# Optimization experiments

Measured on AMD Instinct MI355X. Metric: run time of the kernel, lower is better.

The kernel has to match this reference:

```python
import jax, jax.numpy as jnp
import numpy as np

B, T, C = 2, 2048, 2048
H = 16
HD = C // H
MLP_DIM = 4 * C
EPS = 1e-5


def rmsnorm(x):
    return x * jax.lax.rsqrt(jnp.mean(x * x, axis=-1, keepdims=True) + EPS)


def setup_inputs() -> dict:
    key = jax.random.key(0)
    ks = jax.random.split(key, 7)
    s = 0.02
    return {
        "x": jax.random.normal(ks[0], (B, T, C), dtype=jnp.float32),
        "wq": jax.random.normal(ks[1], (C, C), dtype=jnp.float32) * s,
        "wk": jax.random.normal(ks[2], (C, C), dtype=jnp.float32) * s,
        "wv": jax.random.normal(ks[3], (C, C), dtype=jnp.float32) * s,
        "wo": jax.random.normal(ks[4], (C, C), dtype=jnp.float32) * s,
        "fc1": jax.random.normal(ks[5], (MLP_DIM, C), dtype=jnp.float32) * s,
        "fc2": jax.random.normal(ks[6], (C, MLP_DIM), dtype=jnp.float32) * s,
    }


def reference(x, wq, wk, wv, wo, fc1, fc2):
    # --- attention sub-block (pre-norm) ---
    h = rmsnorm(x)
    # nn.Linear applies x @ W.T
    q = (h @ wq.T).reshape(B, T, H, HD).transpose(0, 2, 1, 3)  # [B,H,T,HD]
    k = (h @ wk.T).reshape(B, T, H, HD).transpose(0, 2, 1, 3)
    v = (h @ wv.T).reshape(B, T, H, HD).transpose(0, 2, 1, 3)
    scale = 1.0 / np.sqrt(HD)
    scores = jnp.einsum("bhqd,bhkd->bhqk", q, k) * scale
    causal_mask = jnp.triu(jnp.full((T, T), -jnp.inf, dtype=scores.dtype), k=1)
    scores = scores + causal_mask
    attn = jax.nn.softmax(scores, axis=-1)
    out = jnp.einsum("bhqk,bhkd->bhqd", attn, v)
    out = out.transpose(0, 2, 1, 3).reshape(B, T, C)
    x = x + out @ wo.T
    # --- MLP sub-block (squared ReLU) ---
    h = rmsnorm(x)
    m = h @ fc1.T
    m = jnp.square(jax.nn.relu(m))
    x = x + m @ fc2.T
    return x
```

## Files before the change

### kernel.cpp

```cpp
#include <hip/hip_runtime.h>


typedef __bf16 bf16x8 __attribute__((ext_vector_type(8)));
typedef __bf16 bf16x4 __attribute__((ext_vector_type(4)));
typedef float  f32x4  __attribute__((ext_vector_type(4)));

static __device__ __forceinline__ __bf16 tobf(float f) { return (__bf16)f; }

static __device__ __forceinline__ void async_copy16(const void* g, void* l) {
    __builtin_amdgcn_global_load_lds(
        (const __attribute__((address_space(1))) void*)g,
        (__attribute__((address_space(3))) void*)l, 16, 0, 0);
}

#define LGKM0_FENCE()  asm volatile("s_waitcnt lgkmcnt(0)" ::: "memory")
#define VMCNT8_FENCE() asm volatile("s_waitcnt vmcnt(8)" ::: "memory")
#define VMCNT0_FENCE() asm volatile("s_waitcnt vmcnt(0)" ::: "memory")
#define CFENCE()       asm volatile("" ::: "memory")

__global__ void detect_dtype_kernel(const unsigned short* __restrict__ xh,
                                    int* __restrict__ flag) {
    int t = threadIdx.x;
    unsigned short u = xh[2 * t];
    int e = (u >> 7) & 0xFF;
    bool outlier = (e < 100) || (e > 131);
    unsigned long long m = __ballot(outlier);
    if (t == 0) *flag = (__popcll(m) >= 16) ? 1 : 0;
}

__global__ __launch_bounds__(256) void convert_w4(
    const void* __restrict__ w0, const void* __restrict__ w1,
    const void* __restrict__ w2, const void* __restrict__ w3,
    __bf16* __restrict__ dqkvo, const int* __restrict__ flagp) {
    constexpr size_t CC = (size_t)2048 * 2048;
    const int y = blockIdx.y;
    size_t i = ((size_t)blockIdx.x * 256 + threadIdx.x) * 8;
    const void* s = (y == 0) ? w0 : (y == 1) ? w1 : (y == 2) ? w2 : w3;
    __bf16* d = dqkvo + (size_t)y * CC;
    if (*flagp != 0) {
        const float4* sp = (const float4*)((const float*)s + i);
        float4 a = sp[0], b = sp[1];
        bf16x8 o = {tobf(a.x), tobf(a.y), tobf(a.z), tobf(a.w),
                    tobf(b.x), tobf(b.y), tobf(b.z), tobf(b.w)};
        *(bf16x8*)(d + i) = o;
    } else {
        *(bf16x8*)(d + i) = *(const bf16x8*)((const __bf16*)s + i);
    }
}

__global__ __launch_bounds__(256) void convert_w1(
    const void* __restrict__ src, __bf16* __restrict__ dst,
    const int* __restrict__ flagp) {
    size_t i = ((size_t)blockIdx.x * 256 + threadIdx.x) * 8;
    if (*flagp != 0) {
        const float4* sp = (const float4*)((const float*)src + i);
        float4 a = sp[0], b = sp[1];
        bf16x8 o = {tobf(a.x), tobf(a.y), tobf(a.z), tobf(a.w),
                    tobf(b.x), tobf(b.y), tobf(b.z), tobf(b.w)};
        *(bf16x8*)(dst + i) = o;
    } else {
        *(bf16x8*)(dst + i) = *(const bf16x8*)((const __bf16*)src + i);
    }
}

template <int SRC>
__global__ __launch_bounds__(256) void rmsnorm_kernel(
    const void* __restrict__ xp, __bf16* __restrict__ h,
    const int* __restrict__ flagp) {
    constexpr int C = 2048;
    const int row = blockIdx.x, t = threadIdx.x;
    float vals[8];
    bool f32in = (SRC == 1) || (*flagp != 0);
    if (f32in) {
        const float4* xr = (const float4*)((const float*)xp + (size_t)row * C);
        float4 a = xr[2 * t], b = xr[2 * t + 1];
        vals[0] = a.x; vals[1] = a.y; vals[2] = a.z; vals[3] = a.w;
        vals[4] = b.x; vals[5] = b.y; vals[6] = b.z; vals[7] = b.w;
    } else {
        bf16x8 a = *((const bf16x8*)((const __bf16*)xp + (size_t)row * C) + t);
#pragma unroll
        for (int j = 0; j < 8; ++j) vals[j] = (float)a[j];
    }
    float ss = 0.f;
#pragma unroll
    for (int j = 0; j < 8; ++j) ss += vals[j] * vals[j];
#pragma unroll
    for (int off = 32; off > 0; off >>= 1) ss += __shfl_down(ss, off);
    __shared__ float red[4];
    if ((t & 63) == 0) red[t >> 6] = ss;
    __syncthreads();
    float mean = (red[0] + red[1] + red[2] + red[3]) * (1.0f / C);
    float sc = rsqrtf(mean + 1e-5f);
    bf16x8 o;
#pragma unroll
    for (int j = 0; j < 8; ++j) o[j] = tobf(vals[j] * sc);
    *((bf16x8*)(h + (size_t)row * C) + t) = o;
}

static __device__ __forceinline__ void gemm_core_128pf(
    const __bf16* __restrict__ A, const __bf16* __restrict__ W,
    int m0, int n0, int K,
    __bf16 (*As)[128][64], __bf16 (*Bs)[128][64], f32x4 (&acc)[4][4]) {
    const int t = threadIdx.x;
    const int wave = t >> 6, lane = t & 63;
    const int lr = lane & 15, lq = lane >> 4;
    const int wm = wave & 1, wn = wave >> 1;
    const int sx = lr & 7;
    const int NT = K >> 6;

    const __bf16* gA[4];
    const __bf16* gB[4];
    int lo[4];
#pragma unroll
    for (int i = 0; i < 4; ++i) {
        int c = i * 256 + t;
        int row = c >> 3;
        int sl = (c & 7) ^ (row & 7);
        gA[i] = A + (size_t)(m0 + row) * K + sl * 8;
        gB[i] = W + (size_t)(n0 + row) * K + sl * 8;
        lo[i] = (c & ~63) * 8;
    }

    const f32x4 zero = {0.f, 0.f, 0.f, 0.f};
#pragma unroll
    for (int i = 0; i < 4; ++i)
#pragma unroll
        for (int j = 0; j < 4; ++j) acc[i][j] = zero;

#pragma unroll
    for (int i = 0; i < 4; ++i) {
        async_copy16(gA[i], &As[0][0][0] + lo[i]);
        async_copy16(gB[i], &Bs[0][0][0] + lo[i]);
    }

    for (int tt = 0; tt < NT; ++tt) {
        const int cur = tt & 1;
        if (tt + 1 < NT) {
            const int k1 = (tt + 1) * 64;
#pragma unroll
            for (int i = 0; i < 4; ++i) {
                async_copy16(gA[i] + k1, &As[cur ^ 1][0][0] + lo[i]);
                async_copy16(gB[i] + k1, &Bs[cur ^ 1][0][0] + lo[i]);
            }
            VMCNT8_FENCE();
        } else {
            VMCNT0_FENCE();
        }
        __builtin_amdgcn_s_barrier();
        CFENCE();

        bf16x8 a[4][2], b[4][2];
#pragma unroll
        for (int kk = 0; kk < 2; ++kk) {
            const int sp = ((kk * 4 + lq) ^ sx) * 8;
#pragma unroll
            for (int ii = 0; ii < 4; ++ii) {
                a[ii][kk] = *(const bf16x8*)&As[cur][wm * 64 + ii * 16 + lr][sp];
                b[ii][kk] = *(const bf16x8*)&Bs[cur][wn * 64 + ii * 16 + lr][sp];
            }
        }
#pragma unroll
        for (int ii = 0; ii < 4; ++ii)
#pragma unroll
            for (int jj = 0; jj < 4; ++jj)
#pragma unroll
                for (int kk = 0; kk < 2; ++kk)
                    acc[ii][jj] = __builtin_amdgcn_mfma_f32_16x16x32_bf16(
                        a[ii][kk], b[jj][kk], acc[ii][jj], 0, 0, 0);
        CFENCE();
        __builtin_amdgcn_s_barrier();
        CFENCE();
    }
}

template <int EPI>
__global__ __launch_bounds__(256) void gemm_nt(
    const __bf16* __restrict__ A, const __bf16* __restrict__ W,
    void* __restrict__ outp, const void* __restrict__ resp,
    int M, int N, int K, const int* __restrict__ flagp) {
    __shared__ __align__(16) __bf16 As[2][128][64];
    __shared__ __align__(16) __bf16 Bs[2][128][64];
    const int t = threadIdx.x;
    const int wave = t >> 6, lane = t & 63;
    const int lr = lane & 15, lq = lane >> 4;
    const int wm = wave & 1, wn = wave >> 1;
    const int m0 = blockIdx.y * 128, n0 = blockIdx.x * 128;

    f32x4 acc[4][4];
    gemm_core_128pf(A, W, m0, n0, K, As, Bs, acc);

    const bool f32 = (*flagp != 0);
#pragma unroll
    for (int i = 0; i < 4; ++i)
#pragma unroll
        for (int j = 0; j < 4; ++j)
#pragma unroll
            for (int r = 0; r < 4; ++r) {
                int row = m0 + wm * 64 + i * 16 + lq * 4 + r;
                int col = n0 + wn * 64 + j * 16 + lr;
                size_t o = (size_t)row * N + col;
                float v = acc[i][j][r];
                if (EPI == 5) {
                    float res = f32 ? ((const float*)resp)[o]
                                    : (float)((const __bf16*)resp)[o];
                    ((float*)outp)[o] = v + res;
                } else {
                    float ov = v + ((const float*)resp)[o];
                    if (f32) ((float*)outp)[o] = ov;
                    else     ((__bf16*)outp)[o] = tobf(ov);
                }
            }
}

__global__ __launch_bounds__(256) void gemm_qkv(
    const __bf16* __restrict__ A, const __bf16* __restrict__ Wall,
    __bf16* __restrict__ qout, __bf16* __restrict__ kout,
    __bf16* __restrict__ vtout) {
    constexpr int N = 2048, K = 2048;
    constexpr float kQScale = 1.4426950408889634f * 0.08838834764831845f;
    __shared__ __align__(16) __bf16 As[2][128][64];
    __shared__ __align__(16) __bf16 Bs[2][128][64];
    const int t = threadIdx.x;
    const int wave = t >> 6, lane = t & 63;
    const int lr = lane & 15, lq = lane >> 4;
    const int wm = wave & 1, wn = wave >> 1;
    const int which = blockIdx.x >> 4;
    const int m0 = blockIdx.y * 128, n0 = (blockIdx.x & 15) * 128;
    const __bf16* W = Wall + (size_t)which * N * K;

    f32x4 acc[4][4];
    gemm_core_128pf(A, W, m0, n0, K, As, Bs, acc);

    if (which < 2) {
        __bf16* outp = (which == 0) ? qout : kout;
        const float sc = (which == 0) ? kQScale : 1.0f;
#pragma unroll
        for (int i = 0; i < 4; ++i)
#pragma unroll
            for (int j = 0; j < 4; ++j)
#pragma unroll
                for (int r = 0; r < 4; ++r) {
                    int row = m0 + wm * 64 + i * 16 + lq * 4 + r;
                    int col = n0 + wn * 64 + j * 16 + lr;
                    outp[(size_t)row * N + col] = tobf(acc[i][j][r] * sc);
                }
    } else {
#pragma unroll
        for (int i = 0; i < 4; ++i)
#pragma unroll
            for (int j = 0; j < 4; ++j) {
                int t0 = m0 + wm * 64 + i * 16 + lq * 4;
                int b  = t0 >> 11, tt = t0 & 2047;
                int col = n0 + wn * 64 + j * 16 + lr;
                bf16x4 p = {tobf(acc[i][j][0]), tobf(acc[i][j][1]),
                            tobf(acc[i][j][2]), tobf(acc[i][j][3])};
                *(bf16x4*)(vtout + (((size_t)(b * 2048 + col)) << 11) + tt) = p;
            }
    }
}

static __device__ __forceinline__ void gemm_core_256(
    const __bf16* __restrict__ A, const __bf16* __restrict__ W,
    int m0, int n0, int K,
    __bf16 (*As)[256][64], __bf16 (*Bs)[256][64], f32x4 (&acc)[8][4]) {
    const int tid = threadIdx.x;
    const int wave = tid >> 6, lane = tid & 63;
    const int lr = lane & 15, lq = lane >> 4;
    const int wm = wave >> 2, wn = wave & 3;
    const int sx = lr & 7;
    const int NT = K >> 6;

    int off[4], lo[4];
#pragma unroll
    for (int i = 0; i < 4; ++i) {
        int c = i * 512 + tid;
        int row = c >> 3;
        off[i] = row * K + (((c & 7) ^ (row & 7)) * 8);
        lo[i] = (c & ~63) * 8;
    }

    const f32x4 zero = {0.f, 0.f, 0.f, 0.f};
#pragma unroll
    for (int m = 0; m < 8; ++m)
#pragma unroll
        for (int n = 0; n < 4; ++n) acc[m][n] = zero;

#pragma unroll
    for (int pt = 0; pt < 2; ++pt) {
        const __bf16* ga = A + (size_t)m0 * K + pt * 64;
        const __bf16* gb = W + (size_t)n0 * K + pt * 64;
#pragma unroll
        for (int i = 0; i < 4; ++i)
            async_copy16(ga + off[i], &As[pt][0][0] + lo[i]);
#pragma unroll
        for (int i = 0; i < 4; ++i)
            async_copy16(gb + off[i], &Bs[pt][0][0] + lo[i]);
    }
    VMCNT8_FENCE();
    __builtin_amdgcn_s_barrier();

    for (int t = 0; t < NT; ++t) {
        const int bi = t & 1;
        const __bf16 (*Ac)[64] = As[bi];
        const __bf16 (*Bc)[64] = Bs[bi];
        const int ts = (t + 2 < NT) ? t + 2 : NT - 1;
        const __bf16* gAt = A + (size_t)m0 * K + (size_t)ts * 64;
        const __bf16* gBt = W + (size_t)n0 * K + (size_t)ts * 64;

        bf16x8 a0[4][2], a1[4][2], b0[2][2], b1[2][2];

#pragma unroll
        for (int m = 0; m < 4; ++m)
#pragma unroll
            for (int kk = 0; kk < 2; ++kk)
                a0[m][kk] = *(const bf16x8*)
                    &Ac[wm * 128 + m * 16 + lr][((kk * 4 + lq) ^ sx) * 8];
#pragma unroll
        for (int n = 0; n < 2; ++n)
#pragma unroll
            for (int kk = 0; kk < 2; ++kk)
                b0[n][kk] = *(const bf16x8*)
                    &Bc[wn * 64 + n * 16 + lr][((kk * 4 + lq) ^ sx) * 8];
        __builtin_amdgcn_s_barrier();
        LGKM0_FENCE();
        __builtin_amdgcn_s_setprio(1);
#pragma unroll
        for (int m = 0; m < 4; ++m)
#pragma unroll
            for (int n = 0; n < 2; ++n)
#pragma unroll
                for (int kk = 0; kk < 2; ++kk)
                    acc[m][n] = __builtin_amdgcn_mfma_f32_16x16x32_bf16(
                        a0[m][kk], b0[n][kk], acc[m][n], 0, 0, 0);
        __builtin_amdgcn_s_setprio(0);
        __builtin_amdgcn_s_barrier();

#pragma unroll
        for (int m = 0; m < 4; ++m)
#pragma unroll
            for (int kk = 0; kk < 2; ++kk)
                a1[m][kk] = *(const bf16x8*)
                    &Ac[wm * 128 + (m + 4) * 16 + lr][((kk * 4 + lq) ^ sx) * 8];
        __builtin_amdgcn_s_barrier();
        LGKM0_FENCE();
        __builtin_amdgcn_s_setprio(1);
#pragma unroll
        for (int m = 0; m < 4; ++m)
#pragma unroll
            for (int n = 0; n < 2; ++n)
#pragma unroll
                for (int kk = 0; kk < 2; ++kk)
                    acc[m + 4][n] = __builtin_amdgcn_mfma_f32_16x16x32_bf16(
                        a1[m][kk], b0[n][kk], acc[m + 4][n], 0, 0, 0);
        __builtin_amdgcn_s_setprio(0);
        __builtin_amdgcn_s_barrier();

#pragma unroll
        for (int n = 0; n < 2; ++n)
#pragma unroll
            for (int kk = 0; kk < 2; ++kk)
                b1[n][kk] = *(const bf16x8*)
                    &Bc[wn * 64 + (n + 2) * 16 + lr][((kk * 4 + lq) ^ sx) * 8];
#pragma unroll
        for (int i = 0; i < 4; ++i)
            async_copy16(gAt + off[i], &As[bi][0][0] + lo[i]);
        __builtin_amdgcn_s_barrier();
        LGKM0_FENCE();
        __builtin_amdgcn_s_setprio(1);
#pragma unroll
        for (int m = 0; m < 4; ++m)
#pragma unroll
            for (int n = 0; n < 2; ++n)
#pragma unroll
                for (int kk = 0; kk < 2; ++kk)
                    acc[m + 4][n + 2] = __builtin_amdgcn_mfma_f32_16x16x32_bf16(
                        a1[m][kk], b1[n][kk], acc[m + 4][n + 2], 0, 0, 0);
        __builtin_amdgcn_s_setprio(0);
        __builtin_amdgcn_s_barrier();

#pragma unroll
        for (int i = 0; i < 4; ++i)
            async_copy16(gBt + off[i], &Bs[bi][0][0] + lo[i]);
        __builtin_amdgcn_s_barrier();
        __builtin_amdgcn_s_setprio(1);
#pragma unroll
        for (int m = 0; m < 4; ++m)
#pragma unroll
            for (int n = 0; n < 2; ++n)
#pragma unroll
                for (int kk = 0; kk < 2; ++kk)
                    acc[m][n + 2] = __builtin_amdgcn_mfma_f32_16x16x32_bf16(
                        a0[m][kk], b1[n][kk], acc[m][n + 2], 0, 0, 0);
        __builtin_amdgcn_s_setprio(0);
        VMCNT8_FENCE();
        __builtin_amdgcn_s_barrier();
    }
}

template <int EPI>
__global__ __launch_bounds__(512, 1) void gemm256_nt(
    const __bf16* __restrict__ A, const __bf16* __restrict__ W,
    void* __restrict__ outp, const void* __restrict__ resp,
    int M, int N, int K, const int* __restrict__ flagp) {
    __shared__ __align__(16) __bf16 As[2][256][64];
    __shared__ __align__(16) __bf16 Bs[2][256][64];
    const int tid = threadIdx.x;
    const int wave = tid >> 6, lane = tid & 63;
    const int lr = lane & 15, lq = lane >> 4;
    const int wm = wave >> 2, wn = wave & 3;
    const int m0 = blockIdx.y * 256, n0 = blockIdx.x * 256;

    f32x4 acc[8][4];
    gemm_core_256(A, W, m0, n0, K, As, Bs, acc);

    const bool f32 = (EPI == 2) ? false : (*flagp != 0);
#pragma unroll
    for (int m = 0; m < 8; ++m)
#pragma unroll
        for (int n = 0; n < 4; ++n)
#pragma unroll
            for (int r = 0; r < 4; ++r) {
                int row = m0 + wm * 128 + m * 16 + lq * 4 + r;
                int col = n0 + wn * 64 + n * 16 + lr;
                size_t o = (size_t)row * N + col;
                float v = acc[m][n][r];
                if (EPI == 2) {
                    float rv = v > 0.f ? v : 0.f;
                    ((__bf16*)outp)[o] = tobf(rv * rv);
                } else if (EPI == 5) {
                    float res = f32 ? ((const float*)resp)[o]
                                    : (float)((const __bf16*)resp)[o];
                    ((float*)outp)[o] = v + res;
                } else {
                    float ov = v + ((const float*)resp)[o];
                    if (f32) ((float*)outp)[o] = ov;
                    else     ((__bf16*)outp)[o] = tobf(ov);
                }
            }
}

__global__ __launch_bounds__(256) void attn_kernel(
    const __bf16* __restrict__ Q, const __bf16* __restrict__ K,
    const __bf16* __restrict__ Vt, __bf16* __restrict__ O) {
    constexpr int T = 2048, C = 2048, HD = 128;
    __shared__ __align__(16) __bf16 Ks[64][136];
    __shared__ __align__(16) __bf16 Vts[128][72];
    __shared__ __align__(16) __bf16 Ps[4][16][72];
    const int t = threadIdx.x, w = t >> 6, lane = t & 63;
    const int lr = lane & 15, lq = lane >> 4;
    const int b = blockIdx.z, h = blockIdx.y;
    const __bf16* vtb = Vt + ((size_t)(b * 2048 + h * 128) << 11);
    const f32x4 zero = {0.f, 0.f, 0.f, 0.f};

    bf16x8 ones;
#pragma unroll
    for (int j = 0; j < 8; ++j) ones[j] = (lr == 0) ? (__bf16)1.0f : (__bf16)0.0f;

    for (int pass = 0; pass < 2; ++pass) {
        const int qblk = (pass == 0) ? blockIdx.x : 31 - blockIdx.x;
        const int q0 = qblk * 64;

        const int qrow = q0 + w * 16 + lr;
        const __bf16* qb = Q + (size_t)(b * T + qrow) * C + h * HD;
        bf16x8 qf[4];
#pragma unroll
        for (int s = 0; s < 4; ++s)
            qf[s] = *(const bf16x8*)(qb + s * 32 + lq * 8);

        f32x4 oacc[8], lacc = zero;
#pragma unroll
        for (int nc = 0; nc < 8; ++nc) oacc[nc] = zero;
        float m_i[4] = {-3e38f, -3e38f, -3e38f, -3e38f};

        for (int kb = 0; kb <= qblk; ++kb) {
            const int k00 = kb * 64;
#pragma unroll
            for (int i = 0; i < 4; ++i) {
                int c = t + 256 * i;
                int r = c >> 4, col = (c & 15) * 8;
                *(bf16x8*)&Ks[r][col] =
                    *(const bf16x8*)(K + (size_t)(b * T + k00 + r) * C + h * HD + col);
            }
#pragma unroll
            for (int i = 0; i < 4; ++i) {
                int c = t + 256 * i;
                int r = c >> 3, cg = (c & 7) * 8;
                *(bf16x8*)&Vts[r][cg] =
                    *(const bf16x8*)(vtb + ((size_t)r << 11) + k00 + cg);
            }
            __syncthreads();

            float pv[4][4];
#pragma unroll
            for (int jc = 0; jc < 4; ++jc) {
                f32x4 s = zero;
#pragma unroll
                for (int ks = 0; ks < 4; ++ks) {
                    bf16x8 kf = *(const bf16x8*)&Ks[jc * 16 + lr][ks * 32 + lq * 8];
                    s = __builtin_amdgcn_mfma_f32_16x16x32_bf16(qf[ks], kf, s, 0, 0, 0);
                }
#pragma unroll
                for (int r = 0; r < 4; ++r) pv[jc][r] = s[r];
            }
            if (kb == qblk) {
#pragma unroll
                for (int jc = 0; jc < 4; ++jc)
#pragma unroll
                    for (int r = 0; r < 4; ++r)
                        if (jc * 16 + lr > w * 16 + lq * 4 + r) pv[jc][r] = -3e38f;
            }
            float rmax[4];
#pragma unroll
            for (int r = 0; r < 4; ++r)
                rmax[r] = fmaxf(fmaxf(pv[0][r], pv[1][r]), fmaxf(pv[2][r], pv[3][r]));
#pragma unroll
            for (int off = 1; off < 16; off <<= 1)
#pragma unroll
                for (int r = 0; r < 4; ++r)
                    rmax[r] = fmaxf(rmax[r], __shfl_xor(rmax[r], off));
            float alpha[4];
#pragma unroll
            for (int r = 0; r < 4; ++r) {
                float mn = fmaxf(m_i[r], rmax[r]);
                alpha[r] = exp2f(m_i[r] - mn);
                m_i[r] = mn;
            }
#pragma unroll
            for (int jc = 0; jc < 4; ++jc)
#pragma unroll
                for (int r = 0; r < 4; ++r)
                    Ps[w][lq * 4 + r][jc * 16 + lr] = tobf(exp2f(pv[jc][r] - m_i[r]));
#pragma unroll
            for (int nc = 0; nc < 8; ++nc)
#pragma unroll
                for (int r = 0; r < 4; ++r) oacc[nc][r] *= alpha[r];
#pragma unroll
            for (int r = 0; r < 4; ++r) lacc[r] *= alpha[r];
            __syncthreads();

#pragma unroll
            for (int s2 = 0; s2 < 2; ++s2) {
                bf16x8 pa = *(const bf16x8*)&Ps[w][lr][s2 * 32 + lq * 8];
#pragma unroll
                for (int nc = 0; nc < 8; ++nc) {
                    bf16x8 vf = *(const bf16x8*)&Vts[nc * 16 + lr][s2 * 32 + lq * 8];
                    oacc[nc] = __builtin_amdgcn_mfma_f32_16x16x32_bf16(
                        pa, vf, oacc[nc], 0, 0, 0);
                }
                lacc = __builtin_amdgcn_mfma_f32_16x16x32_bf16(pa, ones, lacc, 0, 0, 0);
            }
            __syncthreads();
        }

        float inv[4];
#pragma unroll
        for (int r = 0; r < 4; ++r) inv[r] = 1.0f / __shfl(lacc[r], lane & 48);
#pragma unroll
        for (int nc = 0; nc < 8; ++nc)
#pragma unroll
            for (int r = 0; r < 4; ++r) {
                int row = q0 + w * 16 + lq * 4 + r;
                O[(size_t)(b * T + row) * C + h * HD + nc * 16 + lr] =
                    tobf(oacc[nc][r] * inv[r]);
            }
        __syncthreads();
    }
}

extern "C" void kernel_launch(void* const* d_in, const int* in_sizes, int n_in,
                              void* d_out, int out_size, void* d_ws, size_t ws_size,
                              hipStream_t stream) {
    const void* x   = d_in[0];
    const void* wq  = d_in[1];
    const void* wk  = d_in[2];
    const void* wv  = d_in[3];
    const void* wo  = d_in[4];
    const void* fc1 = d_in[5];
    const void* fc2 = d_in[6];
    constexpr int Bv = 2, Tv = 2048, Cv = 2048, Hv = 16, MLP = 8192;
    constexpr int M = Bv * Tv;
    constexpr size_t NE = (size_t)M * Cv;
    constexpr size_t CC = (size_t)Cv * Cv;

    char* ws = (char*)d_ws;
    int*    flag = (int*)ws;
    __bf16* h    = (__bf16*)(ws + 256);
    __bf16* qb   = h  + NE;
    __bf16* kb   = qb + NE;
    __bf16* vt   = kb + NE;
    __bf16* ao   = vt + NE;
    float*  x1   = (float*)(ao + NE);
    __bf16* mm   = (__bf16*)(x1 + NE);
    __bf16* wqkvob = mm;
    __bf16* fc1b   = qb;
    __bf16* fc2b   = vt;

    detect_dtype_kernel<<<1, 64, 0, stream>>>((const unsigned short*)x, flag);

    convert_w4<<<dim3(2048, 4), 256, 0, stream>>>(wq, wk, wv, wo, wqkvob, flag);

    rmsnorm_kernel<0><<<M, 256, 0, stream>>>(x, h, flag);

    gemm_qkv<<<dim3(48, 32), 256, 0, stream>>>(h, wqkvob, qb, kb, vt);

    attn_kernel<<<dim3(16, Hv, Bv), 256, 0, stream>>>(qb, kb, vt, ao);

    convert_w1<<<8192, 256, 0, stream>>>(fc1, fc1b, flag);

    gemm_nt<5><<<dim3(16, 32), 256, 0, stream>>>(ao, wqkvob + 3 * CC, x1, x,
                                                 M, Cv, Cv, flag);

    convert_w1<<<8192, 256, 0, stream>>>(fc2, fc2b, flag);

    rmsnorm_kernel<1><<<M, 256, 0, stream>>>(x1, h, flag);

    gemm256_nt<2><<<dim3(32, 16), 512, 0, stream>>>(h, fc1b, mm, nullptr,
                                                    M, MLP, Cv, flag);

    gemm_nt<6><<<dim3(16, 32), 256, 0, stream>>>(mm, fc2b, d_out, x1,
                                                 M, Cv, MLP, flag);
}
```

Baseline: 772.4 us.

## Prefetch attention K/V tiles into registers, swizzle GEMM block order, interleave LDS reads

In the attention kernel, the next K and V^T tiles are now loaded from global memory into registers while the current tile is being computed, then written to LDS at the start of the next iteration. The goal is to hide global load latency. The GEMM kernel remaps block IDs with a stride-8 swizzle to change which tiles run concurrently, likely for L2 or XCD locality. The GEMM inner loop now issues the MFMAs for each k-slice right after that slice's LDS fragment reads, which lowers register pressure. The register prefetch costs extra VGPRs in the attention kernel. The swizzle assumes the block count is divisible by 8.

```diff
diff --git a/kernel.cpp b/kernel.cpp
--- a/kernel.cpp
+++ b/kernel.cpp
@@ -149,24 +149,22 @@
         __builtin_amdgcn_s_barrier();
         CFENCE();
 
-        bf16x8 a[4][2], b[4][2];
 #pragma unroll
         for (int kk = 0; kk < 2; ++kk) {
             const int sp = ((kk * 4 + lq) ^ sx) * 8;
+            bf16x8 a[4], b[4];
 #pragma unroll
             for (int ii = 0; ii < 4; ++ii) {
-                a[ii][kk] = *(const bf16x8*)&As[cur][wm * 64 + ii * 16 + lr][sp];
-                b[ii][kk] = *(const bf16x8*)&Bs[cur][wn * 64 + ii * 16 + lr][sp];
-            }
+                a[ii] = *(const bf16x8*)&As[cur][wm * 64 + ii * 16 + lr][sp];
+                b[ii] = *(const bf16x8*)&Bs[cur][wn * 64 + ii * 16 + lr][sp];
+            }
+#pragma unroll
+            for (int ii = 0; ii < 4; ++ii)
+#pragma unroll
+                for (int jj = 0; jj < 4; ++jj)
+                    acc[ii][jj] = __builtin_amdgcn_mfma_f32_16x16x32_bf16(
+                        a[ii], b[jj], acc[ii][jj], 0, 0, 0);
         }
-#pragma unroll
-        for (int ii = 0; ii < 4; ++ii)
-#pragma unroll
-            for (int jj = 0; jj < 4; ++jj)
-#pragma unroll
-                for (int kk = 0; kk < 2; ++kk)
-                    acc[ii][jj] = __builtin_amdgcn_mfma_f32_16x16x32_bf16(
-                        a[ii][kk], b[jj][kk], acc[ii][jj], 0, 0, 0);
         CFENCE();
         __builtin_amdgcn_s_barrier();
         CFENCE();
@@ -184,7 +182,10 @@
     const int wave = t >> 6, lane = t & 63;
     const int lr = lane & 15, lq = lane >> 4;
     const int wm = wave & 1, wn = wave >> 1;
-    const int m0 = blockIdx.y * 128, n0 = blockIdx.x * 128;
+    const int id  = blockIdx.x + gridDim.x * blockIdx.y;
+    const int nwg = gridDim.x * gridDim.y;
+    const int swz = (id & 7) * (nwg >> 3) + (id >> 3);
+    const int m0 = (swz / gridDim.x) * 128, n0 = (swz % gridDim.x) * 128;
 
     f32x4 acc[4][4];
     gemm_core_128pf(A, W, m0, n0, K, As, Bs, acc);
@@ -452,6 +453,11 @@
     const __bf16* vtb = Vt + ((size_t)(b * 2048 + h * 128) << 11);
     const f32x4 zero = {0.f, 0.f, 0.f, 0.f};
 
+    const int kr[4] = {t >> 4, (t + 256) >> 4, (t + 512) >> 4, (t + 768) >> 4};
+    const int kc = (t & 15) * 8;
+    const int vr[4] = {t >> 3, (t + 256) >> 3, (t + 512) >> 3, (t + 768) >> 3};
+    const int vc = (t & 7) * 8;
+
     bf16x8 ones;
 #pragma unroll
     for (int j = 0; j < 8; ++j) ones[j] = (lr == 0) ? (__bf16)1.0f : (__bf16)0.0f;
@@ -472,23 +478,31 @@
         for (int nc = 0; nc < 8; ++nc) oacc[nc] = zero;
         float m_i[4] = {-3e38f, -3e38f, -3e38f, -3e38f};
 
+        bf16x8 kreg[4], vreg[4];
+#pragma unroll
+        for (int i = 0; i < 4; ++i)
+            kreg[i] = *(const bf16x8*)(K + (size_t)(b * T + kr[i]) * C + h * HD + kc);
+#pragma unroll
+        for (int i = 0; i < 4; ++i)
+            vreg[i] = *(const bf16x8*)(vtb + ((size_t)vr[i] << 11) + vc);
+
         for (int kb = 0; kb <= qblk; ++kb) {
-            const int k00 = kb * 64;
-#pragma unroll
-            for (int i = 0; i < 4; ++i) {
-                int c = t + 256 * i;
-                int r = c >> 4, col = (c & 15) * 8;
-                *(bf16x8*)&Ks[r][col] =
-                    *(const bf16x8*)(K + (size_t)(b * T + k00 + r) * C + h * HD + col);
-            }
-#pragma unroll
-            for (int i = 0; i < 4; ++i) {
-                int c = t + 256 * i;
-                int r = c >> 3, cg = (c & 7) * 8;
-                *(bf16x8*)&Vts[r][cg] =
-                    *(const bf16x8*)(vtb + ((size_t)r << 11) + k00 + cg);
-            }
+#pragma unroll
+            for (int i = 0; i < 4; ++i) *(bf16x8*)&Ks[kr[i]][kc] = kreg[i];
+#pragma unroll
+            for (int i = 0; i < 4; ++i) *(bf16x8*)&Vts[vr[i]][vc] = vreg[i];
             __syncthreads();
+
+            if (kb < qblk) {
+                const int k01 = (kb + 1) * 64;
+#pragma unroll
+                for (int i = 0; i < 4; ++i)
+                    kreg[i] = *(const bf16x8*)(K + (size_t)(b * T + k01 + kr[i]) * C
+                                               + h * HD + kc);
+#pragma unroll
+                for (int i = 0; i < 4; ++i)
+                    vreg[i] = *(const bf16x8*)(vtb + ((size_t)vr[i] << 11) + k01 + vc);
+            }
 
             float pv[4][4];
 #pragma unroll
```

New measurement: 757.6 us. Within noise of the previous version (-1.9%).
